# Kernel optimization log

Hardware: AMD Instinct MI355X
Metric: run time of the kernel (lower is better)

The kernel has to match this reference:

```python
import jax, jax.numpy as jnp
import numpy as np

H = 1024
S = 8192
B = 1  # module's broadcast in the weighted-sum step only supports B == 1


def setup_inputs() -> dict:
    key = jax.random.key(0)
    k1, k2, k3 = jax.random.split(key, 3)
    scale = 1.0 / np.sqrt(H)
    enc_out = jax.random.normal(k1, (B, S, H), dtype=jnp.float32)
    w1 = jax.random.normal(k2, (H, H), dtype=jnp.float32) * scale  # nn.Linear weight [out,in]
    w2 = jax.random.normal(k3, (H, H), dtype=jnp.float32) * scale
    return {"enc_out": enc_out, "w1": w1, "w2": w2}


def reference(enc_out, w1, w2):
    # attn_weights = tanh(w1(enc_out)) @ w2(enc_out)^T  -> [B, S, S]
    q = jnp.tanh(jnp.einsum('bsh,oh->bso', enc_out, w1))
    k = jnp.einsum('bsh,oh->bso', enc_out, w2)
    scores = jnp.einsum('bih,bjh->bij', q, k)          # [B, S, S]
    attn = jax.nn.softmax(scores, axis=1)               # softmax over dim=1 (rows)
    # torch: sum over dim=1 of attn[B,S,S,1] * enc_out broadcast as [1,B,S,H].
    # For B==1 this equals enc_out[0,j,h] * sum_i attn[0,i,j]; avoid the
    # [B,S,S,H] intermediate the eager torch code materializes.
    col_sum = jnp.sum(attn, axis=1)                     # [B, S]
    context = col_sum[..., None] * enc_out              # [B, S, H]
    return context, attn
```

## Files before the change

### kernel.cpp

```cpp
#include <hip/hip_runtime.h>
#include <hip/hip_bf16.h>
#include <math.h>


typedef _Float16 half_t;
typedef _Float16 half8 __attribute__((ext_vector_type(8)));
typedef _Float16 half4 __attribute__((ext_vector_type(4)));
typedef float f32x4 __attribute__((ext_vector_type(4)));

#define S_DIM 8192
#define H_DIM 1024

__device__ __forceinline__ void gload16(const void* g, void* l) {
  __builtin_amdgcn_global_load_lds(
      (const __attribute__((address_space(1))) void*)g,
      (__attribute__((address_space(3))) void*)l, 16, 0, 0);
}

__global__ void __launch_bounds__(256) k_cvt(const float* __restrict__ src,
                                             half_t* __restrict__ dst) {
  long g = (long)blockIdx.x * 256 + threadIdx.x;
  f32x4 x = ((const f32x4*)src)[g];
  half4 h;
#pragma unroll
  for (int e = 0; e < 4; ++e) h[e] = (half_t)x[e];
  ((half4*)dst)[g] = h;
}

#define GEMM_MAINLOOP(APTR, BPTR)                                              \
  __shared__ half_t As[8192];                                                  \
  __shared__ half_t Bs[8192];                                                  \
  const int tid = threadIdx.x;                                                 \
  const int lane = tid & 63;                                                   \
  const int quad = lane >> 4;                                                  \
  const int l15 = lane & 15;                                                   \
  const int wave = tid >> 6;                                                   \
  const int wm = wave & 1;                                                     \
  const int wn = wave >> 1;                                                    \
  const int bm = blockIdx.y;                                                   \
  const int bn = blockIdx.x;                                                   \
  int aoff[4], boff[4], loff[4];                                               \
  _Pragma("unroll") for (int t = 0; t < 4; ++t) {                              \
    int f8 = t * 256 + tid;                                                    \
    int u = f8 >> 7;                                                           \
    int m = f8 & 127;                                                          \
    aoff[t] = (bm * 128 + m) * H_DIM + u * 8;                                  \
    boff[t] = (bn * 128 + m) * H_DIM + u * 8;                                  \
    loff[t] = f8 * 8;                                                          \
  }                                                                            \
  f32x4 acc[4][4];                                                             \
  _Pragma("unroll") for (int r = 0; r < 4; ++r)                                \
      _Pragma("unroll") for (int c = 0; c < 4; ++c)                            \
          acc[r][c] = (f32x4){0.f, 0.f, 0.f, 0.f};                             \
  for (int k0 = 0; k0 < H_DIM; k0 += 64) {                                     \
    _Pragma("unroll") for (int t = 0; t < 4; ++t)                              \
        gload16(APTR + aoff[t] + k0, &As[loff[t]]);                            \
    _Pragma("unroll") for (int t = 0; t < 4; ++t)                              \
        gload16(BPTR + boff[t] + k0, &Bs[loff[t]]);                            \
    __syncthreads();                                                           \
    _Pragma("unroll") for (int ki = 0; ki < 2; ++ki) {                         \
      const int u = ki * 4 + quad;                                             \
      half8 af[4], bf[4];                                                      \
      _Pragma("unroll") for (int r = 0; r < 4; ++r)                            \
          af[r] = *(const half8*)&As[(u * 128 + wm * 64 + r * 16 + l15) * 8];  \
      _Pragma("unroll") for (int c = 0; c < 4; ++c)                            \
          bf[c] = *(const half8*)&Bs[(u * 128 + wn * 64 + c * 16 + l15) * 8];  \
      _Pragma("unroll") for (int r = 0; r < 4; ++r)                            \
          _Pragma("unroll") for (int c = 0; c < 4; ++c)                        \
              acc[r][c] = __builtin_amdgcn_mfma_f32_16x16x32_f16(              \
                  af[r], bf[c], acc[r][c], 0, 0, 0);                           \
    }                                                                          \
    __syncthreads();                                                           \
  }

__global__ void __launch_bounds__(256) k_gemm_qk(const half_t* __restrict__ A,
                                                 const half_t* __restrict__ B,
                                                 half_t* __restrict__ Qh,
                                                 half_t* __restrict__ Kh) {
  GEMM_MAINLOOP(A, B)
  const int colbase = bn * 128 + wn * 64;
  const int rowb = bm * 128 + wm * 64;
#pragma unroll
  for (int r = 0; r < 4; ++r) {
#pragma unroll
    for (int c = 0; c < 4; ++c) {
      int col = colbase + c * 16 + l15;
      int row = rowb + r * 16 + quad * 4;
#pragma unroll
      for (int v = 0; v < 4; ++v) {
        float x = acc[r][c][v];
        if (col < 1024) {
          Qh[(long)(row + v) * 1024 + col] = (half_t)tanhf(x);
        } else {
          Kh[(long)(row + v) * 1024 + (col - 1024)] = (half_t)x;
        }
      }
    }
  }
}

__global__ void __launch_bounds__(256) k_gemm_scores(const half_t* __restrict__ A,
                                                     const half_t* __restrict__ B,
                                                     float* __restrict__ out) {
  GEMM_MAINLOOP(A, B)
  const int colbase = bn * 128 + wn * 64;
  const int rowb = bm * 128 + wm * 64;
#pragma unroll
  for (int r = 0; r < 4; ++r) {
#pragma unroll
    for (int c = 0; c < 4; ++c) {
      int col = colbase + c * 16 + l15;
      int row = rowb + r * 16 + quad * 4;
#pragma unroll
      for (int v = 0; v < 4; ++v) {
        out[(long)(row + v) * S_DIM + col] = acc[r][c][v];
      }
    }
  }
}

__global__ void __launch_bounds__(256) k_colstats(const float* __restrict__ P,
                                                  float* __restrict__ Pm,
                                                  float* __restrict__ Ps) {
  const int c = threadIdx.x & 63;
  const int rg = threadIdx.x >> 6;
  const int j = blockIdx.x * 64 + c;
  const int seg = blockIdx.y;
  float m = -3.0e38f, s = 0.f;
  for (int t = 0; t < 256; ++t) {
    int i = seg * 1024 + t * 4 + rg;
    float x = P[(long)i * S_DIM + j];
    float mn = fmaxf(m, x);
    s = s * __expf(m - mn) + __expf(x - mn);
    m = mn;
  }
  __shared__ float sm[4][64];
  __shared__ float ss[4][64];
  sm[rg][c] = m;
  ss[rg][c] = s;
  __syncthreads();
  if (threadIdx.x < 64) {
    float mm = sm[0][c];
#pragma unroll
    for (int r = 1; r < 4; ++r) mm = fmaxf(mm, sm[r][c]);
    float sum = 0.f;
#pragma unroll
    for (int r = 0; r < 4; ++r) sum += ss[r][c] * __expf(sm[r][c] - mm);
    Pm[seg * S_DIM + j] = mm;
    Ps[seg * S_DIM + j] = sum;
  }
}

__global__ void __launch_bounds__(256) k_combine(const float* __restrict__ Pm,
                                                 const float* __restrict__ Ps,
                                                 float* __restrict__ Mcol,
                                                 float* __restrict__ Rcol) {
  int j = blockIdx.x * 256 + threadIdx.x;
  float m = Pm[j];
#pragma unroll
  for (int r = 1; r < 8; ++r) m = fmaxf(m, Pm[r * S_DIM + j]);
  float s = 0.f;
#pragma unroll
  for (int r = 0; r < 8; ++r) s += Ps[r * S_DIM + j] * __expf(Pm[r * S_DIM + j] - m);
  Mcol[j] = m;
  Rcol[j] = 1.0f / s;
}

__global__ void __launch_bounds__(256) k_norm(float* __restrict__ P,
                                              const float* __restrict__ Mcol,
                                              const float* __restrict__ Rcol) {
  long gid = (long)blockIdx.x * 256 + threadIdx.x;
  int j4 = (int)(gid & 2047);
  f32x4 x = ((const f32x4*)P)[gid];
  f32x4 a = ((const f32x4*)Mcol)[j4];
  f32x4 r = ((const f32x4*)Rcol)[j4];
  f32x4 o;
#pragma unroll
  for (int e = 0; e < 4; ++e) o[e] = __expf(x[e] - a[e]) * r[e];
  ((f32x4*)P)[gid] = o;
}

__global__ void __launch_bounds__(256) k_copy(const f32x4* __restrict__ src,
                                              f32x4* __restrict__ dst) {
  long g = (long)blockIdx.x * 256 + threadIdx.x;
  dst[g] = src[g];
}

extern "C" void kernel_launch(void* const* d_in, const int* in_sizes, int n_in,
                              void* d_out, int out_size, void* d_ws, size_t ws_size,
                              hipStream_t stream) {
  const float* enc = (const float*)d_in[0];
  const float* w1 = (const float*)d_in[1];
  const float* w2 = (const float*)d_in[2];

  float* out = (float*)d_out;
  float* ctx = out;
  float* attn = out + 8388608;

  half_t* Qh = (half_t*)ctx;
  half_t* Kh = Qh + 8388608;
  half_t* enc_h = (half_t*)attn;
  half_t* w_h = (half_t*)((char*)attn + 16777216);

  char* ws = (char*)d_ws;
  float* Pm = (float*)ws;
  float* Ps = (float*)(ws + 262144);
  float* Mcol = (float*)(ws + 524288);
  float* Rcol = (float*)(ws + 557056);

  k_cvt<<<8192, 256, 0, stream>>>(enc, enc_h);
  k_cvt<<<1024, 256, 0, stream>>>(w1, w_h);
  k_cvt<<<1024, 256, 0, stream>>>(w2, w_h + 1048576);

  k_gemm_qk<<<dim3(16, 64), 256, 0, stream>>>(enc_h, w_h, Qh, Kh);

  k_gemm_scores<<<dim3(64, 64), 256, 0, stream>>>(Qh, Kh, attn);

  k_colstats<<<dim3(128, 8), 256, 0, stream>>>(attn, Pm, Ps);
  k_combine<<<32, 256, 0, stream>>>(Pm, Ps, Mcol, Rcol);
  k_norm<<<65536, 256, 0, stream>>>(attn, Mcol, Rcol);

  k_copy<<<8192, 256, 0, stream>>>((const f32x4*)enc, (f32x4*)ctx);
}
```

Baseline: 770.0 us.

## Fuse column softmax stats into scores GEMM epilogue, swizzle blocks, merge copy into norm

```diff
diff --git a/kernel.cpp b/kernel.cpp
--- a/kernel.cpp
+++ b/kernel.cpp
@@ -37,8 +37,6 @@
   const int wave = tid >> 6;                                                   \
   const int wm = wave & 1;                                                     \
   const int wn = wave >> 1;                                                    \
-  const int bm = blockIdx.y;                                                   \
-  const int bn = blockIdx.x;                                                   \
   int aoff[4], boff[4], loff[4];                                               \
   _Pragma("unroll") for (int t = 0; t < 4; ++t) {                              \
     int f8 = t * 256 + tid;                                                    \
@@ -77,6 +75,8 @@
                                                  const half_t* __restrict__ B,
                                                  half_t* __restrict__ Qh,
                                                  half_t* __restrict__ Kh) {
+  const int bm = blockIdx.y;
+  const int bn = blockIdx.x;
   GEMM_MAINLOOP(A, B)
   const int colbase = bn * 128 + wn * 64;
   const int rowb = bm * 128 + wm * 64;
@@ -99,9 +99,17 @@
   }
 }
 
+template <bool FUSE_STATS>
 __global__ void __launch_bounds__(256) k_gemm_scores(const half_t* __restrict__ A,
                                                      const half_t* __restrict__ B,
-                                                     float* __restrict__ out) {
+                                                     float* __restrict__ out,
+                                                     float* __restrict__ Pm,
+                                                     float* __restrict__ Ps) {
+  const int lin = blockIdx.x;
+  const int patch = lin >> 6;
+  const int local = lin & 63;
+  const int bm = (patch >> 3) * 8 + (local >> 3);
+  const int bn = (patch & 7) * 8 + (local & 7);
   GEMM_MAINLOOP(A, B)
   const int colbase = bn * 128 + wn * 64;
   const int rowb = bm * 128 + wm * 64;
@@ -114,6 +122,52 @@
 #pragma unroll
       for (int v = 0; v < 4; ++v) {
         out[(long)(row + v) * S_DIM + col] = acc[r][c][v];
+      }
+    }
+  }
+  if (FUSE_STATS) {
+    float cmax[4], csum[4];
+#pragma unroll
+    for (int c = 0; c < 4; ++c) {
+      float m = acc[0][c][0];
+#pragma unroll
+      for (int r = 0; r < 4; ++r)
+#pragma unroll
+        for (int v = 0; v < 4; ++v) m = fmaxf(m, acc[r][c][v]);
+      m = fmaxf(m, __shfl_xor(m, 16, 64));
+      m = fmaxf(m, __shfl_xor(m, 32, 64));
+      cmax[c] = m;
+      float s = 0.f;
+#pragma unroll
+      for (int r = 0; r < 4; ++r)
+#pragma unroll
+        for (int v = 0; v < 4; ++v) s += __expf(acc[r][c][v] - m);
+      s += __shfl_xor(s, 16, 64);
+      s += __shfl_xor(s, 32, 64);
+      csum[c] = s;
+    }
+    float* sred = (float*)As;
+    if (quad == 0) {
+#pragma unroll
+      for (int c = 0; c < 4; ++c) {
+        int idx = ((((wm * 2 + wn) * 4 + c) * 16 + l15) * 2);
+        sred[idx] = cmax[c];
+        sred[idx + 1] = csum[c];
+      }
+    }
+    __syncthreads();
+    if (wm == 0 && quad == 0) {
+#pragma unroll
+      for (int c = 0; c < 4; ++c) {
+        int i0 = ((((0 * 2 + wn) * 4 + c) * 16 + l15) * 2);
+        int i1 = ((((1 * 2 + wn) * 4 + c) * 16 + l15) * 2);
+        float m0 = sred[i0], s0 = sred[i0 + 1];
+        float m1 = sred[i1], s1 = sred[i1 + 1];
+        float M = fmaxf(m0, m1);
+        float Ssum = s0 * __expf(m0 - M) + s1 * __expf(m1 - M);
+        int col = colbase + c * 16 + l15;
+        Pm[(long)bm * S_DIM + col] = M;
+        Ps[(long)bm * S_DIM + col] = Ssum;
       }
     }
   }
@@ -154,22 +208,30 @@
 __global__ void __launch_bounds__(256) k_combine(const float* __restrict__ Pm,
                                                  const float* __restrict__ Ps,
                                                  float* __restrict__ Mcol,
-                                                 float* __restrict__ Rcol) {
+                                                 float* __restrict__ Rcol,
+                                                 int nseg) {
   int j = blockIdx.x * 256 + threadIdx.x;
   float m = Pm[j];
-#pragma unroll
-  for (int r = 1; r < 8; ++r) m = fmaxf(m, Pm[r * S_DIM + j]);
+  for (int r = 1; r < nseg; ++r) m = fmaxf(m, Pm[(long)r * S_DIM + j]);
   float s = 0.f;
-#pragma unroll
-  for (int r = 0; r < 8; ++r) s += Ps[r * S_DIM + j] * __expf(Pm[r * S_DIM + j] - m);
+  for (int r = 0; r < nseg; ++r)
+    s += Ps[(long)r * S_DIM + j] * __expf(Pm[(long)r * S_DIM + j] - m);
   Mcol[j] = m;
   Rcol[j] = 1.0f / s;
 }
 
 __global__ void __launch_bounds__(256) k_norm(float* __restrict__ P,
                                               const float* __restrict__ Mcol,
-                                              const float* __restrict__ Rcol) {
-  long gid = (long)blockIdx.x * 256 + threadIdx.x;
+                                              const float* __restrict__ Rcol,
+                                              const f32x4* __restrict__ enc,
+                                              f32x4* __restrict__ ctx) {
+  long b = blockIdx.x;
+  if (b >= 65536) {
+    long g = (b - 65536) * 256 + threadIdx.x;
+    ctx[g] = enc[g];
+    return;
+  }
+  long gid = b * 256 + threadIdx.x;
   int j4 = (int)(gid & 2047);
   f32x4 x = ((const f32x4*)P)[gid];
   f32x4 a = ((const f32x4*)Mcol)[j4];
@@ -178,12 +240,6 @@
 #pragma unroll
   for (int e = 0; e < 4; ++e) o[e] = __expf(x[e] - a[e]) * r[e];
   ((f32x4*)P)[gid] = o;
-}
-
-__global__ void __launch_bounds__(256) k_copy(const f32x4* __restrict__ src,
-                                              f32x4* __restrict__ dst) {
-  long g = (long)blockIdx.x * 256 + threadIdx.x;
-  dst[g] = src[g];
 }
 
 extern "C" void kernel_launch(void* const* d_in, const int* in_sizes, int n_in,
@@ -202,11 +258,13 @@
   half_t* enc_h = (half_t*)attn;
   half_t* w_h = (half_t*)((char*)attn + 16777216);
 
+  const bool fuse = ws_size >= (size_t)(64 + 64 + 2) * S_DIM * 4;
+  const int nseg = fuse ? 64 : 8;
   char* ws = (char*)d_ws;
   float* Pm = (float*)ws;
-  float* Ps = (float*)(ws + 262144);
-  float* Mcol = (float*)(ws + 524288);
-  float* Rcol = (float*)(ws + 557056);
+  float* Ps = (float*)(ws + (size_t)nseg * S_DIM * 4);
+  float* Mcol = (float*)(ws + (size_t)2 * nseg * S_DIM * 4);
+  float* Rcol = Mcol + S_DIM;
 
   k_cvt<<<8192, 256, 0, stream>>>(enc, enc_h);
   k_cvt<<<1024, 256, 0, stream>>>(w1, w_h);
@@ -214,11 +272,14 @@
 
   k_gemm_qk<<<dim3(16, 64), 256, 0, stream>>>(enc_h, w_h, Qh, Kh);
 
-  k_gemm_scores<<<dim3(64, 64), 256, 0, stream>>>(Qh, Kh, attn);
-
-  k_colstats<<<dim3(128, 8), 256, 0, stream>>>(attn, Pm, Ps);
-  k_combine<<<32, 256, 0, stream>>>(Pm, Ps, Mcol, Rcol);
-  k_norm<<<65536, 256, 0, stream>>>(attn, Mcol, Rcol);
-
-  k_copy<<<8192, 256, 0, stream>>>((const f32x4*)enc, (f32x4*)ctx);
-}
+  if (fuse) {
+    k_gemm_scores<true><<<4096, 256, 0, stream>>>(Qh, Kh, attn, Pm, Ps);
+  } else {
+    k_gemm_scores<false><<<4096, 256, 0, stream>>>(Qh, Kh, attn, Pm, Ps);
+    k_colstats<<<dim3(128, 8), 256, 0, stream>>>(attn, Pm, Ps);
+  }
+  k_combine<<<32, 256, 0, stream>>>(Pm, Ps, Mcol, Rcol, nseg);
+
+  k_norm<<<73728, 256, 0, stream>>>(attn, Mcol, Rcol, (const f32x4*)enc,
+                                    (f32x4*)ctx);
+}
```

After: 768.3 us. No clear change (-0.2%).
